# Performance work log

Measured on AMD Instinct MI355X. Metric: run time of the kernel, lower is better.

The kernel has to match this reference:

```python
import jax, jax.numpy as jnp
import numpy as np

N = 50000
E = 1600000
D_IN = 128
D_OUT = 128


def setup_inputs() -> dict:
    key = jax.random.key(0)
    k1, k2, k3, k4, k5 = jax.random.split(key, 5)
    feature = jax.random.normal(k1, (N, D_IN), dtype=jnp.float32)
    src = jax.random.randint(k2, (E,), 0, N, dtype=jnp.int32)
    dst = jax.random.randint(k3, (E,), 0, N, dtype=jnp.int32)
    # nn.Linear(in_feats, out_feats): weight [out, in], bias [out]
    bound = 1.0 / np.sqrt(D_IN)
    weight = jax.random.uniform(k4, (D_OUT, D_IN), minval=-bound, maxval=bound, dtype=jnp.float32)
    bias = jax.random.uniform(k5, (D_OUT,), minval=-bound, maxval=bound, dtype=jnp.float32)
    return {"feature": feature, "src": src, "dst": dst, "weight": weight, "bias": bias}


def reference(feature, src, dst, weight, bias):
    # message: copy src node feature along each edge; reduce: mean over incoming edges
    msgs = feature[src]                              # [E, D_IN] irregular gather
    summed = jax.ops.segment_sum(msgs, dst, num_segments=N)          # [N, D_IN]
    deg = jax.ops.segment_sum(jnp.ones((E,), dtype=feature.dtype), dst, num_segments=N)  # [N]
    # DGL update_all: zero-in-degree nodes keep their original 'h' (feature)
    mean = summed / jnp.maximum(deg, 1.0)[:, None]
    h = jnp.where((deg > 0)[:, None], mean, feature)  # [N, D_IN]
    out = h @ weight.T + bias                          # Linear
    return jax.nn.relu(out)
```

## Files before the change

### kernel.cpp

```cpp
#include <hip/hip_runtime.h>


#define NN 50000
#define EE 1600000
#define DD 128
#define NSTRIP 3125
#define GSB 196
#define CH2 4096
#define NW2 391
#define NPBLK 98
#define NFB 6250
#define NCNT (GSB * NW2)
#define NSA 75
#define WCAP 12288

typedef __attribute__((ext_vector_type(8))) short bf16x8;
typedef __attribute__((ext_vector_type(8))) unsigned short u16x8;
typedef __attribute__((ext_vector_type(4))) float f32x4;

static __device__ __forceinline__ short f2bf(float f) {
  union { float f; unsigned u; } x; x.f = f;
  unsigned r = (x.u + 0x7FFF + ((x.u >> 16) & 1)) >> 16;
  return (short)(r & 0xFFFF);
}

__global__ __launch_bounds__(256) void k1(
    const int* __restrict__ dst, int* __restrict__ cnt2,
    const float* __restrict__ feature, unsigned short* __restrict__ fb) {
  if (blockIdx.x < NPBLK) {
    __shared__ int cnt[4][GSB];
    const int wv = threadIdx.x >> 6, lane = threadIdx.x & 63;
    const int w = blockIdx.x * 4 + wv;
    const bool act = (w < NW2);
    for (int i = lane; i < GSB; i += 64) cnt[wv][i] = 0;
    __syncthreads();
    if (act) {
      const int base = w * CH2;
#pragma unroll 4
      for (int it = 0; it < 16; ++it) {
        int e0 = base + it * 256 + lane * 4;
        if (e0 < EE) {
          int4 d4 = *(const int4*)(dst + e0);
          atomicAdd(&cnt[wv][((unsigned)d4.x) >> 8], 1);
          atomicAdd(&cnt[wv][((unsigned)d4.y) >> 8], 1);
          atomicAdd(&cnt[wv][((unsigned)d4.z) >> 8], 1);
          atomicAdd(&cnt[wv][((unsigned)d4.w) >> 8], 1);
        }
      }
    }
    __syncthreads();
    if (act) {
      for (int i = lane; i < GSB; i += 64) cnt2[i * NW2 + w] = cnt[wv][i];
    }
  } else {
    int i = (blockIdx.x - NPBLK) * 256 + threadIdx.x;
    if (i < NN * DD / 4) {
      float4 v = ((const float4*)feature)[i];
      short4 o;
      o.x = f2bf(v.x); o.y = f2bf(v.y); o.z = f2bf(v.z); o.w = f2bf(v.w);
      ((short4*)fb)[i] = o;
    }
  }
}

__global__ __launch_bounds__(1024) void sA_bsum(
    const int* __restrict__ in, int* __restrict__ bsum, int n) {
  __shared__ int ws[16];
  int i = blockIdx.x * 1024 + threadIdx.x;
  int v = (i < n) ? in[i] : 0;
#pragma unroll
  for (int d = 1; d < 64; d <<= 1) v += __shfl_xor(v, d, 64);
  int wv = threadIdx.x >> 6, lane = threadIdx.x & 63;
  if (lane == 0) ws[wv] = v;
  __syncthreads();
  if (threadIdx.x == 0) {
    int s = 0;
#pragma unroll
    for (int k = 0; k < 16; ++k) s += ws[k];
    bsum[blockIdx.x] = s;
  }
}

__global__ __launch_bounds__(1024) void p2_scan(
    const int* __restrict__ in, int* __restrict__ out, int n) {
  __shared__ int ws[16];
  __shared__ int s_off;
  const int wv = threadIdx.x >> 6, lane = threadIdx.x & 63;
  if (threadIdx.x == 0) s_off = 0;
  __syncthreads();
  for (int base = 0; base < n; base += 1024) {
    int i = base + threadIdx.x;
    int v = (i < n) ? in[i] : 0;
    int x = v;
#pragma unroll
    for (int d = 1; d < 64; d <<= 1) { int t = __shfl_up(x, d, 64); if (lane >= d) x += t; }
    if (lane == 63) ws[wv] = x;
    __syncthreads();
    if (threadIdx.x < 16) {
      int w = ws[threadIdx.x];
#pragma unroll
      for (int d = 1; d < 16; d <<= 1) { int t = __shfl_up(w, d, 16); if (threadIdx.x >= d) w += t; }
      ws[threadIdx.x] = w;
    }
    __syncthreads();
    int off = s_off + ((wv == 0) ? 0 : ws[wv - 1]);
    if (i < n) out[i] = off + x - v;
    __syncthreads();
    if (threadIdx.x == 0) s_off += ws[15];
    __syncthreads();
  }
}

__global__ __launch_bounds__(1024) void sC_apply(
    int* __restrict__ data, const int* __restrict__ bsum, int n) {
  __shared__ int ws[16];
  int i = blockIdx.x * 1024 + threadIdx.x;
  int wv = threadIdx.x >> 6, lane = threadIdx.x & 63;
  int v = (i < n) ? data[i] : 0;
  int x = v;
#pragma unroll
  for (int d = 1; d < 64; d <<= 1) { int t = __shfl_up(x, d, 64); if (lane >= d) x += t; }
  if (lane == 63) ws[wv] = x;
  __syncthreads();
  if (threadIdx.x < 16) {
    int w = ws[threadIdx.x];
#pragma unroll
    for (int d = 1; d < 16; d <<= 1) { int t = __shfl_up(w, d, 16); if (threadIdx.x >= d) w += t; }
    ws[threadIdx.x] = w;
  }
  __syncthreads();
  int off = bsum[blockIdx.x] + ((wv == 0) ? 0 : ws[wv - 1]);
  if (i < n) data[i] = off + x - v;
}

__global__ __launch_bounds__(256) void p3b(
    const int* __restrict__ src, const int* __restrict__ dst,
    const int* __restrict__ off2, unsigned int* __restrict__ ss) {
  __shared__ int cur[4][GSB];
  const int wv = threadIdx.x >> 6, lane = threadIdx.x & 63;
  const int w = blockIdx.x * 4 + wv;
  const bool act = (w < NW2);
  if (act) {
    for (int i = lane; i < GSB; i += 64) cur[wv][i] = off2[i * NW2 + w];
  }
  __syncthreads();
  if (act) {
    const int base = w * CH2;
#pragma unroll 2
    for (int it = 0; it < 16; ++it) {
      int e0 = base + it * 256 + lane * 4;
      if (e0 < EE) {
        int4 s4 = *(const int4*)(src + e0);
        int4 d4 = *(const int4*)(dst + e0);
        {
          int p = atomicAdd(&cur[wv][((unsigned)d4.x) >> 8], 1);
          ss[p] = (((unsigned)d4.x) << 16) | (unsigned)s4.x;
        }
        {
          int p = atomicAdd(&cur[wv][((unsigned)d4.y) >> 8], 1);
          ss[p] = (((unsigned)d4.y) << 16) | (unsigned)s4.y;
        }
        {
          int p = atomicAdd(&cur[wv][((unsigned)d4.z) >> 8], 1);
          ss[p] = (((unsigned)d4.z) << 16) | (unsigned)s4.z;
        }
        {
          int p = atomicAdd(&cur[wv][((unsigned)d4.w) >> 8], 1);
          ss[p] = (((unsigned)d4.w) << 16) | (unsigned)s4.w;
        }
      }
    }
  }
}

__global__ __launch_bounds__(1024) void fillL2(
    const unsigned int* __restrict__ ss, const int* __restrict__ off2,
    int* __restrict__ csr, int* __restrict__ row_start) {
  __shared__ int win[WCAP];
  __shared__ int cur[256];
  __shared__ int rs[257];
  __shared__ int wsum2[4];
  const int g    = blockIdx.x;
  const int lo   = g * 256;
  const int nloc = (NN - lo < 256) ? (NN - lo) : 256;
  const int ebase = off2[g * NW2];
  const int eend  = (g < GSB - 1) ? off2[(g + 1) * NW2] : EE;
  const int T = eend - ebase;

  if (threadIdx.x < 256) cur[threadIdx.x] = 0;
  __syncthreads();

  for (int e = ebase + threadIdx.x; e < eend; e += 1024) {
    atomicAdd(&cur[(ss[e] >> 16) & 255], 1);
  }
  __syncthreads();

  int x = 0;
  if (threadIdx.x < 256) {
    const int lane = threadIdx.x & 63;
    x = cur[threadIdx.x];
#pragma unroll
    for (int d = 1; d < 64; d <<= 1) { int t = __shfl_up(x, d, 64); if (lane >= d) x += t; }
    if (lane == 63) wsum2[threadIdx.x >> 6] = x;
  }
  __syncthreads();
  if (threadIdx.x < 256) {
    const int wv2 = threadIdx.x >> 6;
    int pre = 0;
#pragma unroll
    for (int k = 0; k < 4; ++k) pre += (k < wv2) ? wsum2[k] : 0;
    rs[threadIdx.x + 1] = pre + x;
    if (threadIdx.x == 0) rs[0] = 0;
    cur[threadIdx.x] = 0;
  }
  __syncthreads();

  if (threadIdx.x <= nloc) row_start[lo + threadIdx.x] = ebase + rs[threadIdx.x];

  if (T <= WCAP) {
    for (int e = ebase + threadIdx.x; e < eend; e += 1024) {
      unsigned pe = ss[e];
      int li = (pe >> 16) & 255;
      int p = atomicAdd(&cur[li], 1);
      win[rs[li] + p] = (int)(pe & 0xFFFFu);
    }
    __syncthreads();
    for (int i = threadIdx.x; i < T; i += 1024) csr[ebase + i] = win[i];
  } else {
    for (int e = ebase + threadIdx.x; e < eend; e += 1024) {
      unsigned pe = ss[e];
      int li = (pe >> 16) & 255;
      int p = atomicAdd(&cur[li], 1);
      csr[ebase + rs[li] + p] = (int)(pe & 0xFFFFu);
    }
  }
}

__global__ __launch_bounds__(256) void aggregate_bf16(
    const unsigned short* __restrict__ fb,
    const int* __restrict__ row_start,
    const int* __restrict__ csr_src,
    unsigned short* __restrict__ hb) {
  const int wave = threadIdx.x >> 6;
  const int lane = threadIdx.x & 63;
  int n = blockIdx.x * 4 + wave;
  if (n >= NN) return;

  const int start = row_start[n];
  const int end   = row_start[n + 1];
  const int deg   = end - start;
  const int q  = lane >> 4;
  const int sl = lane & 15;

  const u16x8* fp = (const u16x8*)fb;
  float acc[8];
#pragma unroll
  for (int j = 0; j < 8; ++j) acc[j] = 0.f;

#pragma unroll 8
  for (int e = start + q; e < end; e += 4) {
    int s = csr_src[e];
    u16x8 v = fp[(size_t)s * 16 + sl];
#pragma unroll
    for (int j = 0; j < 8; ++j) {
      union { unsigned u; float f; } c; c.u = ((unsigned)v[j]) << 16;
      acc[j] += c.f;
    }
  }
#pragma unroll
  for (int j = 0; j < 8; ++j) {
    acc[j] += __shfl_xor(acc[j], 16, 64);
    acc[j] += __shfl_xor(acc[j], 32, 64);
  }

  if (q == 0) {
    u16x8 hv;
    if (deg > 0) {
      float inv = 1.0f / (float)deg;
#pragma unroll
      for (int j = 0; j < 8; ++j) hv[j] = (unsigned short)f2bf(acc[j] * inv);
    } else {
      hv = fp[(size_t)n * 16 + sl];
    }
    ((u16x8*)hb)[(size_t)n * 16 + sl] = hv;
  }
}

__global__ __launch_bounds__(256) void mfma_gemm2(
    const short* __restrict__ hb,
    const float* __restrict__ weight,
    const float* __restrict__ bias,
    float* __restrict__ out) {
  __shared__ bf16x8 wfrag[2048];
  __shared__ float  bias_l[DD];

#pragma unroll
  for (int k = 0; k < 8; ++k) {
    int idx  = threadIdx.x * 8 + k;
    int ln   = idx & 63;
    int ct   = idx >> 6;
    int c    = ct >> 2;
    int t    = ct & 3;
    const float* wp = weight + (c * 16 + (ln & 15)) * DD + t * 32 + (ln >> 4) * 8;
    float4 w0 = *(const float4*)(wp);
    float4 w1 = *(const float4*)(wp + 4);
    bf16x8 b;
    b[0] = f2bf(w0.x); b[1] = f2bf(w0.y); b[2] = f2bf(w0.z); b[3] = f2bf(w0.w);
    b[4] = f2bf(w1.x); b[5] = f2bf(w1.y); b[6] = f2bf(w1.z); b[7] = f2bf(w1.w);
    wfrag[idx] = b;
  }
  if (threadIdx.x < DD) bias_l[threadIdx.x] = bias[threadIdx.x];
  __syncthreads();

  const int wave = threadIdx.x >> 6;
  const int lane = threadIdx.x & 63;
  const int r  = lane & 15;
  const int g  = lane >> 4;

#pragma unroll
  for (int s = 0; s < 2; ++s) {
    const int strip = blockIdx.x * 8 + wave * 2 + s;
    if (strip >= NSTRIP) continue;
    const int m0 = strip * 16;

    bf16x8 Af[4];
#pragma unroll
    for (int t = 0; t < 4; ++t) {
      Af[t] = *(const bf16x8*)(hb + (size_t)(m0 + r) * DD + t * 32 + g * 8);
    }

#pragma unroll
    for (int c = 0; c < 8; ++c) {
      f32x4 acc = {0.f, 0.f, 0.f, 0.f};
#pragma unroll
      for (int t = 0; t < 4; ++t) {
        acc = __builtin_amdgcn_mfma_f32_16x16x32_bf16(Af[t], wfrag[(c * 4 + t) * 64 + lane], acc, 0, 0, 0);
      }
      const float b = bias_l[c * 16 + r];
#pragma unroll
      for (int q = 0; q < 4; ++q) {
        int row = m0 + g * 4 + q;
        float v = acc[q] + b;
        out[(size_t)row * DD + c * 16 + r] = v > 0.f ? v : 0.f;
      }
    }
  }
}

extern "C" void kernel_launch(void* const* d_in, const int* in_sizes, int n_in,
                              void* d_out, int out_size, void* d_ws, size_t ws_size,
                              hipStream_t stream) {
  const float* feature = (const float*)d_in[0];
  const int*   src     = (const int*)d_in[1];
  const int*   dst     = (const int*)d_in[2];
  const float* weight  = (const float*)d_in[3];
  const float* bias    = (const float*)d_in[4];
  float* out = (float*)d_out;

  int* cnt2      = (int*)d_ws;
  int* bsum      = cnt2 + 76640;
  int* row_start = bsum + 80;
  unsigned short* hb = (unsigned short*)(cnt2 + 126724);

  unsigned int* ss = (unsigned int*)d_out;
  int* csr = (int*)d_out + EE;
  unsigned short* fb = (unsigned short*)((int*)d_out + 2 * EE);

  k1<<<NPBLK + NFB, 256, 0, stream>>>(dst, cnt2, feature, fb);
  sA_bsum<<<NSA, 1024, 0, stream>>>(cnt2, bsum, NCNT);
  p2_scan<<<1, 1024, 0, stream>>>(bsum, bsum, NSA);
  sC_apply<<<NSA, 1024, 0, stream>>>(cnt2, bsum, NCNT);
  p3b<<<NPBLK, 256, 0, stream>>>(src, dst, cnt2, ss);
  fillL2<<<GSB, 1024, 0, stream>>>(ss, cnt2, csr, row_start);
  aggregate_bf16<<<(NN + 3) / 4, 256, 0, stream>>>(fb, row_start, csr, hb);
  mfma_gemm2<<<(NSTRIP + 7) / 8, 256, 0, stream>>>((const short*)hb, weight, bias, out);
}
```

Measured before the change: 123.3 us.

## Fuse CSR fill and aggregation into one kernel using LDS-resident edge lists

Merges the fillL2 CSR construction and the aggregate_bf16 gather into a single kernel. Each 256-node group is now split across two blocks, and each block keeps its half's source indices in LDS and aggregates them directly. This avoids writing the CSR and row_start arrays to global memory and reading them back, and it removes one launch. In exchange, each block re-reads and re-counts the whole group's ss segment. Parallelism is also lower: only 392 blocks of 16 waves each handle the gather, compared with 12500 small blocks before.

After: 108.4 us. -12.1%, faster.

```diff
diff --git a/kernel.cpp b/kernel.cpp
--- a/kernel.cpp
+++ b/kernel.cpp
@@ -12,7 +12,7 @@
 #define NFB 6250
 #define NCNT (GSB * NW2)
 #define NSA 75
-#define WCAP 12288
+#define WCAPH 8192
 
 typedef __attribute__((ext_vector_type(8))) short bf16x8;
 typedef __attribute__((ext_vector_type(8))) unsigned short u16x8;
@@ -173,23 +173,28 @@
   }
 }
 
-__global__ __launch_bounds__(1024) void fillL2(
+__global__ __launch_bounds__(1024) void fillagg(
     const unsigned int* __restrict__ ss, const int* __restrict__ off2,
-    int* __restrict__ csr, int* __restrict__ row_start) {
-  __shared__ int win[WCAP];
+    const unsigned short* __restrict__ fb,
+    int* __restrict__ csr_fb,
+    unsigned short* __restrict__ hb) {
+  __shared__ int win[WCAPH];
   __shared__ int cur[256];
   __shared__ int rs[257];
   __shared__ int wsum2[4];
-  const int g    = blockIdx.x;
+  const int g    = blockIdx.x >> 1;
+  const int half = blockIdx.x & 1;
   const int lo   = g * 256;
-  const int nloc = (NN - lo < 256) ? (NN - lo) : 256;
+  const int nl_all = (NN - lo < 256) ? (NN - lo) : 256;
+  int h0 = half * 128;
+  int h1 = h0 + 128;
+  if (h1 > nl_all) h1 = nl_all;
+  if (h1 < h0) h1 = h0;
   const int ebase = off2[g * NW2];
   const int eend  = (g < GSB - 1) ? off2[(g + 1) * NW2] : EE;
-  const int T = eend - ebase;
 
   if (threadIdx.x < 256) cur[threadIdx.x] = 0;
   __syncthreads();
-
   for (int e = ebase + threadIdx.x; e < eend; e += 1024) {
     atomicAdd(&cur[(ss[e] >> 16) & 255], 1);
   }
@@ -215,74 +220,64 @@
   }
   __syncthreads();
 
-  if (threadIdx.x <= nloc) row_start[lo + threadIdx.x] = ebase + rs[threadIdx.x];
-
-  if (T <= WCAP) {
-    for (int e = ebase + threadIdx.x; e < eend; e += 1024) {
-      unsigned pe = ss[e];
-      int li = (pe >> 16) & 255;
+  const int wb = rs[h0];
+  const int Th = rs[h1] - wb;
+  const bool inlds = (Th <= WCAPH);
+
+  for (int e = ebase + threadIdx.x; e < eend; e += 1024) {
+    unsigned pe = ss[e];
+    int li = (pe >> 16) & 255;
+    if (li >= h0 && li < h1) {
       int p = atomicAdd(&cur[li], 1);
-      win[rs[li] + p] = (int)(pe & 0xFFFFu);
-    }
-    __syncthreads();
-    for (int i = threadIdx.x; i < T; i += 1024) csr[ebase + i] = win[i];
-  } else {
-    for (int e = ebase + threadIdx.x; e < eend; e += 1024) {
-      unsigned pe = ss[e];
-      int li = (pe >> 16) & 255;
-      int p = atomicAdd(&cur[li], 1);
-      csr[ebase + rs[li] + p] = (int)(pe & 0xFFFFu);
-    }
-  }
-}
-
-__global__ __launch_bounds__(256) void aggregate_bf16(
-    const unsigned short* __restrict__ fb,
-    const int* __restrict__ row_start,
-    const int* __restrict__ csr_src,
-    unsigned short* __restrict__ hb) {
-  const int wave = threadIdx.x >> 6;
+      if (inlds) win[rs[li] - wb + p] = (int)(pe & 0xFFFFu);
+      else       csr_fb[ebase + rs[li] + p] = (int)(pe & 0xFFFFu);
+    }
+  }
+  __syncthreads();
+
+  const int wv = threadIdx.x >> 6;
   const int lane = threadIdx.x & 63;
-  int n = blockIdx.x * 4 + wave;
-  if (n >= NN) return;
-
-  const int start = row_start[n];
-  const int end   = row_start[n + 1];
-  const int deg   = end - start;
   const int q  = lane >> 4;
   const int sl = lane & 15;
-
   const u16x8* fp = (const u16x8*)fb;
-  float acc[8];
-#pragma unroll
-  for (int j = 0; j < 8; ++j) acc[j] = 0.f;
-
-#pragma unroll 8
-  for (int e = start + q; e < end; e += 4) {
-    int s = csr_src[e];
-    u16x8 v = fp[(size_t)s * 16 + sl];
+
+  for (int ln = h0 + wv; ln < h1; ln += 16) {
+    const int st = rs[ln];
+    const int en = rs[ln + 1];
+    const int deg = en - st;
+    const int n = lo + ln;
+
+    float acc[8];
+#pragma unroll
+    for (int j = 0; j < 8; ++j) acc[j] = 0.f;
+
+#pragma unroll 4
+    for (int e = st + q; e < en; e += 4) {
+      int s = inlds ? win[e - wb] : csr_fb[ebase + e];
+      u16x8 v = fp[(size_t)s * 16 + sl];
+#pragma unroll
+      for (int j = 0; j < 8; ++j) {
+        union { unsigned u; float f; } c; c.u = ((unsigned)v[j]) << 16;
+        acc[j] += c.f;
+      }
+    }
 #pragma unroll
     for (int j = 0; j < 8; ++j) {
-      union { unsigned u; float f; } c; c.u = ((unsigned)v[j]) << 16;
-      acc[j] += c.f;
-    }
-  }
-#pragma unroll
-  for (int j = 0; j < 8; ++j) {
-    acc[j] += __shfl_xor(acc[j], 16, 64);
-    acc[j] += __shfl_xor(acc[j], 32, 64);
-  }
-
-  if (q == 0) {
-    u16x8 hv;
-    if (deg > 0) {
-      float inv = 1.0f / (float)deg;
-#pragma unroll
-      for (int j = 0; j < 8; ++j) hv[j] = (unsigned short)f2bf(acc[j] * inv);
-    } else {
-      hv = fp[(size_t)n * 16 + sl];
-    }
-    ((u16x8*)hb)[(size_t)n * 16 + sl] = hv;
+      acc[j] += __shfl_xor(acc[j], 16, 64);
+      acc[j] += __shfl_xor(acc[j], 32, 64);
+    }
+
+    if (q == 0) {
+      u16x8 hv;
+      if (deg > 0) {
+        float inv = 1.0f / (float)deg;
+#pragma unroll
+        for (int j = 0; j < 8; ++j) hv[j] = (unsigned short)f2bf(acc[j] * inv);
+      } else {
+        hv = fp[(size_t)n * 16 + sl];
+      }
+      ((u16x8*)hb)[(size_t)n * 16 + sl] = hv;
+    }
   }
 }
 
@@ -357,13 +352,12 @@
   const float* bias    = (const float*)d_in[4];
   float* out = (float*)d_out;
 
-  int* cnt2      = (int*)d_ws;
-  int* bsum      = cnt2 + 76640;
-  int* row_start = bsum + 80;
+  int* cnt2 = (int*)d_ws;
+  int* bsum = cnt2 + 76640;
   unsigned short* hb = (unsigned short*)(cnt2 + 126724);
 
   unsigned int* ss = (unsigned int*)d_out;
-  int* csr = (int*)d_out + EE;
+  int* csr_fb = (int*)d_out + EE;
   unsigned short* fb = (unsigned short*)((int*)d_out + 2 * EE);
 
   k1<<<NPBLK + NFB, 256, 0, stream>>>(dst, cnt2, feature, fb);
@@ -371,7 +365,6 @@
   p2_scan<<<1, 1024, 0, stream>>>(bsum, bsum, NSA);
   sC_apply<<<NSA, 1024, 0, stream>>>(cnt2, bsum, NCNT);
   p3b<<<NPBLK, 256, 0, stream>>>(src, dst, cnt2, ss);
-  fillL2<<<GSB, 1024, 0, stream>>>(ss, cnt2, csr, row_start);
-  aggregate_bf16<<<(NN + 3) / 4, 256, 0, stream>>>(fb, row_start, csr, hb);
+  fillagg<<<GSB * 2, 1024, 0, stream>>>(ss, cnt2, fb, csr_fb, hb);
   mfma_gemm2<<<(NSTRIP + 7) / 8, 256, 0, stream>>>((const short*)hb, weight, bias, out);
 }
```
